# Kernel tuning notes

Hardware: AMD Instinct MI355X
Metric: run time of the kernel (lower is better)

Reference implementation:

```python
import jax, jax.numpy as jnp
import numpy as np

B, S, D, H = 8, 512, 1024, 16
DK = D // H          # 64
N_ASP = 4            # aspect tokens per sample
NEG = -1000000000.0


def setup_inputs() -> dict:
    key = jax.random.key(0)
    ks = jax.random.split(key, 12)
    return {
        "query": jax.random.normal(ks[0], (B, S, D), jnp.float32),
        "key_in": jax.random.normal(ks[1], (B, S, D), jnp.float32),
        "mask": jax.random.randint(ks[2], (B, S, S), 0, 2).astype(jnp.int32),
        "aspect": jax.random.normal(ks[3], (B, 1, D), jnp.float32),
        "aspect_ids": jax.random.randint(ks[4], (B, N_ASP), 0, S),
        # learned params
        "Wq": jax.random.normal(ks[5], (D, D), jnp.float32) / np.sqrt(D).astype(np.float32),
        "bq": jnp.zeros((D,), jnp.float32),
        "Wk": jax.random.normal(ks[6], (D, D), jnp.float32) / np.sqrt(D).astype(np.float32),
        "bk": jnp.zeros((D,), jnp.float32),
        "Wd": jax.random.normal(ks[7], (D, DK), jnp.float32) / np.sqrt(D).astype(np.float32),
        "bd": jnp.zeros((DK,), jnp.float32),
        "weight_m": jax.random.normal(ks[8], (H, DK, DK), jnp.float32) / np.sqrt(DK).astype(np.float32),
        "bias_m": jnp.zeros((1,), jnp.float32),
    }


def reference(query, key_in, mask, aspect, aspect_ids,
              Wq, bq, Wk, bk, Wd, bd, weight_m, bias_m):
    # projections -> [B,H,S,DK]
    q = (query @ Wq + bq).reshape(B, S, H, DK).transpose(0, 2, 1, 3)
    k = (key_in @ Wk + bk).reshape(B, S, H, DK).transpose(0, 2, 1, 3)

    # aspect -> dense -> broadcast to [B,H,S,DK]
    asp = aspect @ Wd + bd                                  # [B,1,DK]
    asp = jnp.broadcast_to(asp[:, None, :, :], (B, H, S, DK))

    # asps = tanh(aspect @ W_m @ K^T + bias_m)  -> [B,H,S,S]
    aw = jnp.einsum('bhsd,hde->bhse', asp, weight_m)
    asps = jnp.tanh(jnp.einsum('bhse,bhte->bhst', aw, k) + bias_m[0])

    # per-(batch,head) average score vector over rows -> [B,H,S]
    avg = asps.sum(axis=-2) / S

    # scatter: for each aspect index, overwrite its row and column with avg
    # (sequential over the small fixed N_ASP, matching torch write order:
    #  row write then column write per index)
    a_sc = asps
    bidx = jnp.arange(B)
    for j in range(N_ASP):
        idx = aspect_ids[:, j]                              # [B]
        a_sc = a_sc.at[bidx, :, idx, :].set(avg)            # rows
        a_sc = a_sc.at[bidx, :, :, idx].set(avg)            # cols

    # standard masked attention probs
    scores = jnp.einsum('bhsd,bhtd->bhst', q, k) / np.float32(np.sqrt(DK))
    scores = jnp.where(mask[:, None, :, :] == 0, NEG, scores)
    attn = jax.nn.softmax(scores, axis=-1)
    return a_sc, attn
```

## Files before the change

### kernel.cpp

```cpp
#include <hip/hip_runtime.h>

typedef __bf16 bf16x8 __attribute__((ext_vector_type(8)));
typedef float  f32x4  __attribute__((ext_vector_type(4)));

__device__ __forceinline__ unsigned short f2bf(float f) {
  union { float f; unsigned u; } x; x.f = f;
  unsigned r = (x.u + 0x7FFFu + ((x.u >> 16) & 1u)) >> 16;
  return (unsigned short)r;
}

__device__ __forceinline__ void gload_lds16(const void* g, void* l) {
  __builtin_amdgcn_global_load_lds((__attribute__((address_space(1))) void*)g,
                                   (__attribute__((address_space(3))) void*)l,
                                   16, 0, 0);
}

__global__ void conv_kernel(const float* __restrict__ a, const float* __restrict__ b,
                            unsigned short* __restrict__ ao, unsigned short* __restrict__ bo,
                            int n4) {
  int i = blockIdx.x * 256 + threadIdx.x;
  if (i < n4) {
    float4 x = ((const float4*)a)[i];
    ushort4 y; y.x = f2bf(x.x); y.y = f2bf(x.y); y.z = f2bf(x.z); y.w = f2bf(x.w);
    ((ushort4*)ao)[i] = y;
  } else {
    int j = i - n4;
    float4 x = ((const float4*)b)[j];
    ushort4 y; y.x = f2bf(x.x); y.y = f2bf(x.y); y.z = f2bf(x.z); y.w = f2bf(x.w);
    ((ushort4*)bo)[j] = y;
  }
}

__global__ void wtrans_kernel(const float* __restrict__ Wq, const float* __restrict__ Wk,
                              unsigned short* __restrict__ Wqt, unsigned short* __restrict__ Wkt) {
  const float* W = blockIdx.z ? Wk : Wq;
  unsigned short* Wt = blockIdx.z ? Wkt : Wqt;
  __shared__ unsigned short tile[32][33];
  int k0 = blockIdx.x * 32, n0 = blockIdx.y * 32;
  int tx = threadIdx.x, ty = threadIdx.y;
  #pragma unroll
  for (int i = 0; i < 4; ++i) {
    int k = ty + i * 8;
    tile[k][tx] = f2bf(W[(size_t)(k0 + k) * 1024 + n0 + tx]);
  }
  __syncthreads();
  #pragma unroll
  for (int i = 0; i < 4; ++i) {
    int n = ty + i * 8;
    Wt[(size_t)(n0 + n) * 1024 + k0 + tx] = tile[tx][n];
  }
}

__global__ __launch_bounds__(256)
void prep_kernel(const float* __restrict__ aspect, const float* __restrict__ Wd,
                 const float* __restrict__ bd, const float* __restrict__ weight_m,
                 const float* __restrict__ Wk, const float* __restrict__ bk,
                 float* __restrict__ u_out, float* __restrict__ c_out) {
  int bh = blockIdx.x, b = bh >> 4, h = bh & 15;
  int tid = threadIdx.x, e = tid & 63, g = tid >> 6;
  __shared__ float part[4][64];
  __shared__ float asp_s[64];
  __shared__ float aw_s[64];
  const float* arow = aspect + (size_t)b * 1024;
  float acc = 0.f;
  for (int d = g * 256; d < g * 256 + 256; ++d)
    acc += arow[d] * Wd[(size_t)d * 64 + e];
  part[g][e] = acc;
  __syncthreads();
  if (tid < 64)
    asp_s[tid] = bd[tid] + part[0][tid] + part[1][tid] + part[2][tid] + part[3][tid];
  __syncthreads();
  if (tid < 64) {
    const float* wm = weight_m + (size_t)h * 4096;
    float aw = 0.f;
    #pragma unroll 8
    for (int d = 0; d < 64; ++d) aw += asp_s[d] * wm[d * 64 + tid];
    aw_s[tid] = aw;
  }
  __syncthreads();
  float awl = aw_s[e];
  if (g == 0) {
    float s = bk[h * 64 + e] * awl;
    #pragma unroll
    for (int off = 32; off >= 1; off >>= 1) s += __shfl_xor(s, off, 64);
    if (e == 0) c_out[bh] = s;
  }
  for (int d0 = g * 2; d0 < 1024; d0 += 8) {
    float s0 = Wk[(size_t)d0 * 1024 + h * 64 + e] * awl;
    float s1 = Wk[(size_t)(d0 + 1) * 1024 + h * 64 + e] * awl;
    #pragma unroll
    for (int off = 32; off >= 1; off >>= 1) {
      s0 += __shfl_xor(s0, off, 64);
      s1 += __shfl_xor(s1, off, 64);
    }
    if (e == 0) {
      u_out[(size_t)bh * 1024 + d0]     = s0;
      u_out[(size_t)bh * 1024 + d0 + 1] = s1;
    }
  }
}

__global__ void bitmask_kernel(const int* __restrict__ mask, unsigned long long* __restrict__ mb) {
  int gw = (blockIdx.x * 256 + threadIdx.x) >> 6;
  int lane = threadIdx.x & 63;
  for (int row = gw; row < 4096; row += 1024) {
    const int* mr = mask + (size_t)row * 512;
    unsigned long long* dst = mb + (size_t)row * 8;
    #pragma unroll
    for (int it = 0; it < 8; ++it) {
      int m = mr[it * 64 + lane];
      unsigned long long bb = __ballot(m != 0);
      if (lane == 0) dst[it] = bb;
    }
  }
}

__global__ __launch_bounds__(256)
void v_kernel(const float* __restrict__ key_in, const float* __restrict__ u,
              const float* __restrict__ c, const float* __restrict__ bias_m,
              float* __restrict__ v) {
  __shared__ float ks_[8][1024];
  int b = blockIdx.y, t0 = blockIdx.x * 8;
  int tid = threadIdx.x, wid = tid >> 6, lane = tid & 63;
  const float4* ksrc = (const float4*)(key_in + ((size_t)b * 512 + t0) * 1024);
  float4* kdst = (float4*)&ks_[0][0];
  for (int i = tid; i < 2048; i += 256) kdst[i] = ksrc[i];
  __syncthreads();
  const float* ub = u + (size_t)b * 16384;
  int r0 = wid * 2;
  float acc0[16] = {}, acc1[16] = {};
  for (int i = 0; i < 16; ++i) {
    int col = lane + 64 * i;
    float kv0 = ks_[r0][col], kv1 = ks_[r0 + 1][col];
    #pragma unroll
    for (int h = 0; h < 16; ++h) {
      float uv = ub[h * 1024 + col];
      acc0[h] += kv0 * uv;
      acc1[h] += kv1 * uv;
    }
  }
  float cb = bias_m[0];
  #pragma unroll
  for (int h = 0; h < 16; ++h) {
    float a0 = acc0[h], a1 = acc1[h];
    #pragma unroll
    for (int off = 32; off >= 1; off >>= 1) {
      a0 += __shfl_xor(a0, off, 64);
      a1 += __shfl_xor(a1, off, 64);
    }
    if (lane == h) {
      int bh = b * 16 + h;
      float cc = c[bh] + cb;
      v[(size_t)bh * 512 + t0 + r0]     = tanhf(a0 + cc);
      v[(size_t)bh * 512 + t0 + r0 + 1] = tanhf(a1 + cc);
    }
  }
}

__global__ void asc_kernel(const float* __restrict__ v, const int* __restrict__ ids,
                           float* __restrict__ out) {
  size_t i4 = (size_t)blockIdx.x * 256 + threadIdx.x;
  int t0 = (int)(i4 & 127) * 4;
  int s  = (int)(i4 >> 7) & 511;
  int bh = (int)(i4 >> 16);
  int b  = bh >> 4;
  int i0 = ids[b * 4], i1 = ids[b * 4 + 1], i2 = ids[b * 4 + 2], i3 = ids[b * 4 + 3];
  #define LASTOF(t) ((i3==(t))?3:(i2==(t))?2:(i1==(t))?1:(i0==(t))?0:-1)
  int ls  = LASTOF(s);
  int lt0 = LASTOF(t0), lt1 = LASTOF(t0+1), lt2 = LASTOF(t0+2), lt3 = LASTOF(t0+3);
  #undef LASTOF
  const float* vrow = v + (size_t)bh * 512;
  float vs = vrow[s];
  float4 vt = *(const float4*)(vrow + t0);
  f32x4 o;
  o[0] = (lt0 >= 0 && lt0 >= ls) ? vs : vt.x;
  o[1] = (lt1 >= 0 && lt1 >= ls) ? vs : vt.y;
  o[2] = (lt2 >= 0 && lt2 >= ls) ? vs : vt.z;
  o[3] = (lt3 >= 0 && lt3 >= ls) ? vs : vt.w;
  __builtin_nontemporal_store(o, ((f32x4*)out) + i4);
}

__global__ __launch_bounds__(256, 2)
void gemm_kernel(const unsigned short* __restrict__ Aq, const unsigned short* __restrict__ Ak,
                 const unsigned short* __restrict__ Bq, const unsigned short* __restrict__ Bk,
                 const float* __restrict__ bq, const float* __restrict__ bk,
                 unsigned short* __restrict__ qb, unsigned short* __restrict__ kb) {
  const unsigned short* A  = blockIdx.z ? Ak : Aq;
  const unsigned short* Bt = blockIdx.z ? Bk : Bq;
  const float* bias = blockIdx.z ? bk : bq;
  unsigned short* out = blockIdx.z ? kb : qb;
  const int m0 = blockIdx.y * 128, n0 = blockIdx.x * 128;
  __shared__ __align__(16) unsigned short As[128 * 32];
  __shared__ __align__(16) unsigned short Bs[128 * 32];
  const int tid = threadIdx.x, wid = tid >> 6, lane = tid & 63;
  const int wr = wid >> 1, wc = wid & 1;
  const int quad = lane >> 4, l15 = lane & 15;
  const int rstage = lane >> 2;
  const int kc = (lane & 3) * 8;
  f32x4 acc[4][4] = {};
  for (int k0 = 0; k0 < 1024; k0 += 32) {
    #pragma unroll
    for (int i = 0; i < 2; ++i) {
      int row = wid * 32 + i * 16 + rstage;
      gload_lds16(A  + (size_t)(m0 + row) * 1024 + k0 + kc, As + (wid * 32 + i * 16) * 32);
      gload_lds16(Bt + (size_t)(n0 + row) * 1024 + k0 + kc, Bs + (wid * 32 + i * 16) * 32);
    }
    __syncthreads();
    bf16x8 af[4], bfr[4];
    #pragma unroll
    for (int mi = 0; mi < 4; ++mi)
      af[mi] = *(const bf16x8*)(As + (wr * 64 + mi * 16 + l15) * 32 + quad * 8);
    #pragma unroll
    for (int ni = 0; ni < 4; ++ni)
      bfr[ni] = *(const bf16x8*)(Bs + (wc * 64 + ni * 16 + l15) * 32 + quad * 8);
    #pragma unroll
    for (int mi = 0; mi < 4; ++mi)
      #pragma unroll
      for (int ni = 0; ni < 4; ++ni)
        acc[mi][ni] = __builtin_amdgcn_mfma_f32_16x16x32_bf16(af[mi], bfr[ni], acc[mi][ni], 0, 0, 0);
    __syncthreads();
  }
  #pragma unroll
  for (int mi = 0; mi < 4; ++mi) {
    #pragma unroll
    for (int ni = 0; ni < 4; ++ni) {
      const int n = n0 + wc * 64 + ni * 16 + l15;
      const int hh = n >> 6, dk = n & 63;
      const float bv = bias[n];
      #pragma unroll
      for (int r = 0; r < 4; ++r) {
        const int m = m0 + wr * 64 + mi * 16 + quad * 4 + r;
        const int bb = m >> 9, ss = m & 511;
        out[(((size_t)bb * 16 + hh) * 512 + ss) * 64 + dk] = f2bf(acc[mi][ni][r] + bv);
      }
    }
  }
}

__global__ __launch_bounds__(256, 2)
void attn_kernel(const unsigned short* __restrict__ qb, const unsigned short* __restrict__ kb,
                 const unsigned* __restrict__ mbits, float* __restrict__ attn) {
  __shared__ __align__(16) unsigned short ks[256 * 64];
  __shared__ __align__(16) unsigned short qs[64 * 64];
  const int s0 = blockIdx.x * 64;
  const int h = blockIdx.y, b = blockIdx.z, bh = b * 16 + h;
  const int tid = threadIdx.x, wid = tid >> 6, lane = tid & 63;
  const int quad = lane >> 4, l15 = lane & 15;
  const unsigned short* kslab = kb + (size_t)bh * 512 * 64;
  const unsigned short* qslab = qb + ((size_t)bh * 512 + s0) * 64;
  #pragma unroll
  for (int i = 0; i < 2; ++i)
    gload_lds16(qslab + (wid * 2 + i) * 512 + lane * 8, qs + (wid * 2 + i) * 512);
  #pragma unroll
  for (int i = 0; i < 8; ++i)
    gload_lds16(kslab + (wid * 8 + i) * 512 + lane * 8, ks + (wid * 8 + i) * 512);
  __syncthreads();
  bf16x8 af0 = *(const bf16x8*)(qs + (wid * 16 + l15) * 64 + quad * 8);
  bf16x8 af1 = *(const bf16x8*)(qs + (wid * 16 + l15) * 64 + 32 + quad * 8);
  f32x4 acc[32];
  #pragma unroll
  for (int tile = 0; tile < 16; ++tile) {
    bf16x8 b0 = *(const bf16x8*)(ks + (tile * 16 + l15) * 64 + quad * 8);
    bf16x8 b1 = *(const bf16x8*)(ks + (tile * 16 + l15) * 64 + 32 + quad * 8);
    f32x4 a = {0.f, 0.f, 0.f, 0.f};
    a = __builtin_amdgcn_mfma_f32_16x16x32_bf16(af0, b0, a, 0, 0, 0);
    a = __builtin_amdgcn_mfma_f32_16x16x32_bf16(af1, b1, a, 0, 0, 0);
    acc[tile] = a;
  }
  __syncthreads();
  #pragma unroll
  for (int i = 0; i < 8; ++i)
    gload_lds16(kslab + 16384 + (wid * 8 + i) * 512 + lane * 8, ks + (wid * 8 + i) * 512);
  __syncthreads();
  #pragma unroll
  for (int tile = 16; tile < 32; ++tile) {
    int tl = tile - 16;
    bf16x8 b0 = *(const bf16x8*)(ks + (tl * 16 + l15) * 64 + quad * 8);
    bf16x8 b1 = *(const bf16x8*)(ks + (tl * 16 + l15) * 64 + 32 + quad * 8);
    f32x4 a = {0.f, 0.f, 0.f, 0.f};
    a = __builtin_amdgcn_mfma_f32_16x16x32_bf16(af0, b0, a, 0, 0, 0);
    a = __builtin_amdgcn_mfma_f32_16x16x32_bf16(af1, b1, a, 0, 0, 0);
    acc[tile] = a;
  }
  const size_t srow = (size_t)s0 + wid * 16 + quad * 4;
  const unsigned* mrow = mbits + ((size_t)b * 512 + srow) * 16;
  float mx[4] = {-3.0e38f, -3.0e38f, -3.0e38f, -3.0e38f};
  #pragma unroll
  for (int tp = 0; tp < 16; ++tp) {
    #pragma unroll
    for (int r = 0; r < 4; ++r) {
      unsigned m = mrow[(size_t)r * 16 + tp];
      float sc0 = acc[2 * tp][r] * 0.125f;
      float sc1 = acc[2 * tp + 1][r] * 0.125f;
      sc0 = ((m >> l15) & 1u) ? sc0 : -1.0e9f;
      sc1 = ((m >> (16 + l15)) & 1u) ? sc1 : -1.0e9f;
      acc[2 * tp][r] = sc0;
      acc[2 * tp + 1][r] = sc1;
      mx[r] = fmaxf(mx[r], fmaxf(sc0, sc1));
    }
  }
  #pragma unroll
  for (int r = 0; r < 4; ++r)
    #pragma unroll
    for (int off = 1; off < 16; off <<= 1)
      mx[r] = fmaxf(mx[r], __shfl_xor(mx[r], off, 64));
  float sm[4] = {0.f, 0.f, 0.f, 0.f};
  #pragma unroll
  for (int tile = 0; tile < 32; ++tile)
    #pragma unroll
    for (int r = 0; r < 4; ++r) {
      float e = __expf(acc[tile][r] - mx[r]);
      acc[tile][r] = e;
      sm[r] += e;
    }
  #pragma unroll
  for (int r = 0; r < 4; ++r) {
    #pragma unroll
    for (int off = 1; off < 16; off <<= 1)
      sm[r] += __shfl_xor(sm[r], off, 64);
    sm[r] = 1.0f / sm[r];
  }
  float* obase = attn + ((size_t)bh * 512 + srow) * 512 + l15;
  #pragma unroll
  for (int r = 0; r < 4; ++r)
    #pragma unroll
    for (int tile = 0; tile < 32; ++tile)
      __builtin_nontemporal_store(acc[tile][r] * sm[r], &obase[(size_t)r * 512 + tile * 16]);
}

extern "C" void kernel_launch(void* const* d_in, const int* in_sizes, int n_in,
                              void* d_out, int out_size, void* d_ws, size_t ws_size,
                              hipStream_t stream) {
  const float* query    = (const float*)d_in[0];
  const float* key_in   = (const float*)d_in[1];
  const int*   mask     = (const int*)d_in[2];
  const float* aspect   = (const float*)d_in[3];
  const int*   a_ids    = (const int*)d_in[4];
  const float* Wq       = (const float*)d_in[5];
  const float* bq       = (const float*)d_in[6];
  const float* Wk       = (const float*)d_in[7];
  const float* bk       = (const float*)d_in[8];
  const float* Wd       = (const float*)d_in[9];
  const float* bd       = (const float*)d_in[10];
  const float* weight_m = (const float*)d_in[11];
  const float* bias_m   = (const float*)d_in[12];

  float* out_asc  = (float*)d_out;
  float* out_attn = out_asc + 33554432ull;

  char* ws = (char*)d_ws;
  unsigned short* Aq   = (unsigned short*)(ws);
  unsigned short* Ak   = (unsigned short*)(ws + 8388608);
  unsigned short* Wqt  = (unsigned short*)(ws + 16777216);
  unsigned short* Wkt  = (unsigned short*)(ws + 18874368);
  unsigned short* qbuf = (unsigned short*)(ws + 20971520);
  unsigned short* kbuf = (unsigned short*)(ws + 29360128);
  float* u   = (float*)(ws + 37748736);
  float* c   = (float*)(ws + 38273024);
  float* v   = (float*)(ws + 38277120);
  unsigned long long* mb = (unsigned long long*)(ws + 38539264);

  conv_kernel<<<dim3(8192), dim3(256), 0, stream>>>(query, key_in, Aq, Ak, 1048576);
  wtrans_kernel<<<dim3(32, 32, 2), dim3(32, 8), 0, stream>>>(Wq, Wk, Wqt, Wkt);
  prep_kernel<<<dim3(128), dim3(256), 0, stream>>>(aspect, Wd, bd, weight_m, Wk, bk, u, c);
  bitmask_kernel<<<dim3(256), dim3(256), 0, stream>>>(mask, mb);
  gemm_kernel<<<dim3(8, 32, 2), dim3(256), 0, stream>>>(Aq, Ak, Wqt, Wkt, bq, bk, qbuf, kbuf);
  v_kernel<<<dim3(64, 8), dim3(256), 0, stream>>>(key_in, u, c, bias_m, v);
  asc_kernel<<<dim3(32768), dim3(256), 0, stream>>>(v, a_ids, out_asc);
  attn_kernel<<<dim3(8, 16, 8), dim3(256), 0, stream>>>(qbuf, kbuf, (const unsigned*)mb, out_attn);
}
```

Baseline: 487.8 us.

## Swizzle LDS layouts, deepen GEMM K-tile, split prep kernel, reorder grids

Splits the serial prep kernel into an aw/c kernel and a separate wide-grid kernel that computes u, so the Wk reduction runs across many blocks instead of 128. The projection GEMM moves to a 64-wide K step with an XOR-swizzled LDS layout to cut bank conflicts and halve the number of barriers. The attention kernel uses the same swizzle for its Q/K tiles. Grid dimensions are reordered in both kernels so blocks that share data run close together. This adds one extra launch and a small workspace buffer, and doubles GEMM LDS use, which may lower occupancy.

```diff
diff --git a/kernel.cpp b/kernel.cpp
--- a/kernel.cpp
+++ b/kernel.cpp
@@ -52,10 +52,10 @@
 }
 
 __global__ __launch_bounds__(256)
-void prep_kernel(const float* __restrict__ aspect, const float* __restrict__ Wd,
-                 const float* __restrict__ bd, const float* __restrict__ weight_m,
-                 const float* __restrict__ Wk, const float* __restrict__ bk,
-                 float* __restrict__ u_out, float* __restrict__ c_out) {
+void prep_aw_kernel(const float* __restrict__ aspect, const float* __restrict__ Wd,
+                    const float* __restrict__ bd, const float* __restrict__ weight_m,
+                    const float* __restrict__ bk,
+                    float* __restrict__ aw_out, float* __restrict__ c_out) {
   int bh = blockIdx.x, b = bh >> 4, h = bh & 15;
   int tid = threadIdx.x, e = tid & 63, g = tid >> 6;
   __shared__ float part[4][64];
@@ -76,16 +76,27 @@
     #pragma unroll 8
     for (int d = 0; d < 64; ++d) aw += asp_s[d] * wm[d * 64 + tid];
     aw_s[tid] = aw;
-  }
-  __syncthreads();
-  float awl = aw_s[e];
+    aw_out[(size_t)bh * 64 + tid] = aw;
+  }
+  __syncthreads();
   if (g == 0) {
-    float s = bk[h * 64 + e] * awl;
+    float s = bk[h * 64 + e] * aw_s[e];
     #pragma unroll
     for (int off = 32; off >= 1; off >>= 1) s += __shfl_xor(s, off, 64);
     if (e == 0) c_out[bh] = s;
   }
-  for (int d0 = g * 2; d0 < 1024; d0 += 8) {
+}
+
+__global__ __launch_bounds__(256)
+void prep_u_kernel(const float* __restrict__ Wk, const float* __restrict__ aw_in,
+                   float* __restrict__ u_out) {
+  int bh = blockIdx.y, h = bh & 15;
+  int dbase = blockIdx.x * 128;
+  int tid = threadIdx.x, e = tid & 63, g = tid >> 6;
+  float awl = aw_in[(size_t)bh * 64 + e];
+  #pragma unroll 4
+  for (int it = 0; it < 16; ++it) {
+    int d0 = dbase + g * 32 + it * 2;
     float s0 = Wk[(size_t)d0 * 1024 + h * 64 + e] * awl;
     float s1 = Wk[(size_t)(d0 + 1) * 1024 + h * 64 + e] * awl;
     #pragma unroll
@@ -189,35 +200,44 @@
   const unsigned short* Bt = blockIdx.z ? Bk : Bq;
   const float* bias = blockIdx.z ? bk : bq;
   unsigned short* out = blockIdx.z ? kb : qb;
-  const int m0 = blockIdx.y * 128, n0 = blockIdx.x * 128;
-  __shared__ __align__(16) unsigned short As[128 * 32];
-  __shared__ __align__(16) unsigned short Bs[128 * 32];
+  const int m0 = blockIdx.x * 128, n0 = blockIdx.y * 128;
+  __shared__ __align__(16) unsigned short As[128 * 64];
+  __shared__ __align__(16) unsigned short Bs[128 * 64];
   const int tid = threadIdx.x, wid = tid >> 6, lane = tid & 63;
   const int wr = wid >> 1, wc = wid & 1;
   const int quad = lane >> 4, l15 = lane & 15;
-  const int rstage = lane >> 2;
-  const int kc = (lane & 3) * 8;
+  const int srw = lane >> 3;
+  const int jcol = ((lane & 7) ^ srw) * 8;
+  const int p0 = (quad ^ (l15 & 7)) * 8;
   f32x4 acc[4][4] = {};
-  for (int k0 = 0; k0 < 1024; k0 += 32) {
-    #pragma unroll
-    for (int i = 0; i < 2; ++i) {
-      int row = wid * 32 + i * 16 + rstage;
-      gload_lds16(A  + (size_t)(m0 + row) * 1024 + k0 + kc, As + (wid * 32 + i * 16) * 32);
-      gload_lds16(Bt + (size_t)(n0 + row) * 1024 + k0 + kc, Bs + (wid * 32 + i * 16) * 32);
+  for (int k0 = 0; k0 < 1024; k0 += 64) {
+    #pragma unroll
+    for (int i = 0; i < 4; ++i) {
+      int r = wid * 32 + i * 8 + srw;
+      gload_lds16(A  + (size_t)(m0 + r) * 1024 + k0 + jcol, As + (wid * 32 + i * 8) * 64);
+      gload_lds16(Bt + (size_t)(n0 + r) * 1024 + k0 + jcol, Bs + (wid * 32 + i * 8) * 64);
     }
     __syncthreads();
-    bf16x8 af[4], bfr[4];
-    #pragma unroll
-    for (int mi = 0; mi < 4; ++mi)
-      af[mi] = *(const bf16x8*)(As + (wr * 64 + mi * 16 + l15) * 32 + quad * 8);
-    #pragma unroll
-    for (int ni = 0; ni < 4; ++ni)
-      bfr[ni] = *(const bf16x8*)(Bs + (wc * 64 + ni * 16 + l15) * 32 + quad * 8);
+    bf16x8 af[4][2], bfr[4][2];
+    #pragma unroll
+    for (int mi = 0; mi < 4; ++mi) {
+      const unsigned short* base = As + (wr * 64 + mi * 16 + l15) * 64;
+      af[mi][0] = *(const bf16x8*)(base + p0);
+      af[mi][1] = *(const bf16x8*)(base + (p0 ^ 32));
+    }
+    #pragma unroll
+    for (int ni = 0; ni < 4; ++ni) {
+      const unsigned short* base = Bs + (wc * 64 + ni * 16 + l15) * 64;
+      bfr[ni][0] = *(const bf16x8*)(base + p0);
+      bfr[ni][1] = *(const bf16x8*)(base + (p0 ^ 32));
+    }
     #pragma unroll
     for (int mi = 0; mi < 4; ++mi)
       #pragma unroll
-      for (int ni = 0; ni < 4; ++ni)
-        acc[mi][ni] = __builtin_amdgcn_mfma_f32_16x16x32_bf16(af[mi], bfr[ni], acc[mi][ni], 0, 0, 0);
+      for (int ni = 0; ni < 4; ++ni) {
+        acc[mi][ni] = __builtin_amdgcn_mfma_f32_16x16x32_bf16(af[mi][0], bfr[ni][0], acc[mi][ni], 0, 0, 0);
+        acc[mi][ni] = __builtin_amdgcn_mfma_f32_16x16x32_bf16(af[mi][1], bfr[ni][1], acc[mi][ni], 0, 0, 0);
+      }
     __syncthreads();
   }
   #pragma unroll
@@ -242,26 +262,31 @@
                  const unsigned* __restrict__ mbits, float* __restrict__ attn) {
   __shared__ __align__(16) unsigned short ks[256 * 64];
   __shared__ __align__(16) unsigned short qs[64 * 64];
-  const int s0 = blockIdx.x * 64;
-  const int h = blockIdx.y, b = blockIdx.z, bh = b * 16 + h;
+  const int bh = blockIdx.x, b = bh >> 4;
+  const int s0 = blockIdx.y * 64;
   const int tid = threadIdx.x, wid = tid >> 6, lane = tid & 63;
   const int quad = lane >> 4, l15 = lane & 15;
+  const int srw = lane >> 3;
+  const int j8 = ((lane & 7) ^ srw) * 8;
+  const int p0 = (quad ^ (l15 & 7)) * 8;
   const unsigned short* kslab = kb + (size_t)bh * 512 * 64;
   const unsigned short* qslab = qb + ((size_t)bh * 512 + s0) * 64;
   #pragma unroll
   for (int i = 0; i < 2; ++i)
-    gload_lds16(qslab + (wid * 2 + i) * 512 + lane * 8, qs + (wid * 2 + i) * 512);
+    gload_lds16(qslab + (wid * 2 + i) * 512 + srw * 64 + j8, qs + (wid * 2 + i) * 512);
   #pragma unroll
   for (int i = 0; i < 8; ++i)
-    gload_lds16(kslab + (wid * 8 + i) * 512 + lane * 8, ks + (wid * 8 + i) * 512);
-  __syncthreads();
-  bf16x8 af0 = *(const bf16x8*)(qs + (wid * 16 + l15) * 64 + quad * 8);
-  bf16x8 af1 = *(const bf16x8*)(qs + (wid * 16 + l15) * 64 + 32 + quad * 8);
+    gload_lds16(kslab + (wid * 8 + i) * 512 + srw * 64 + j8, ks + (wid * 8 + i) * 512);
+  __syncthreads();
+  const unsigned short* qbase = qs + (wid * 16 + l15) * 64;
+  bf16x8 af0 = *(const bf16x8*)(qbase + p0);
+  bf16x8 af1 = *(const bf16x8*)(qbase + (p0 ^ 32));
   f32x4 acc[32];
   #pragma unroll
   for (int tile = 0; tile < 16; ++tile) {
-    bf16x8 b0 = *(const bf16x8*)(ks + (tile * 16 + l15) * 64 + quad * 8);
-    bf16x8 b1 = *(const bf16x8*)(ks + (tile * 16 + l15) * 64 + 32 + quad * 8);
+    const unsigned short* kbase = ks + (tile * 16 + l15) * 64;
+    bf16x8 b0 = *(const bf16x8*)(kbase + p0);
+    bf16x8 b1 = *(const bf16x8*)(kbase + (p0 ^ 32));
     f32x4 a = {0.f, 0.f, 0.f, 0.f};
     a = __builtin_amdgcn_mfma_f32_16x16x32_bf16(af0, b0, a, 0, 0, 0);
     a = __builtin_amdgcn_mfma_f32_16x16x32_bf16(af1, b1, a, 0, 0, 0);
@@ -270,13 +295,13 @@
   __syncthreads();
   #pragma unroll
   for (int i = 0; i < 8; ++i)
-    gload_lds16(kslab + 16384 + (wid * 8 + i) * 512 + lane * 8, ks + (wid * 8 + i) * 512);
+    gload_lds16(kslab + 16384 + (wid * 8 + i) * 512 + srw * 64 + j8, ks + (wid * 8 + i) * 512);
   __syncthreads();
   #pragma unroll
   for (int tile = 16; tile < 32; ++tile) {
-    int tl = tile - 16;
-    bf16x8 b0 = *(const bf16x8*)(ks + (tl * 16 + l15) * 64 + quad * 8);
-    bf16x8 b1 = *(const bf16x8*)(ks + (tl * 16 + l15) * 64 + 32 + quad * 8);
+    const unsigned short* kbase = ks + ((tile - 16) * 16 + l15) * 64;
+    bf16x8 b0 = *(const bf16x8*)(kbase + p0);
+    bf16x8 b1 = *(const bf16x8*)(kbase + (p0 ^ 32));
     f32x4 a = {0.f, 0.f, 0.f, 0.f};
     a = __builtin_amdgcn_mfma_f32_16x16x32_bf16(af0, b0, a, 0, 0, 0);
     a = __builtin_amdgcn_mfma_f32_16x16x32_bf16(af1, b1, a, 0, 0, 0);
@@ -359,13 +384,15 @@
   float* c   = (float*)(ws + 38273024);
   float* v   = (float*)(ws + 38277120);
   unsigned long long* mb = (unsigned long long*)(ws + 38539264);
+  float* aw  = (float*)(ws + 38801408);
 
   conv_kernel<<<dim3(8192), dim3(256), 0, stream>>>(query, key_in, Aq, Ak, 1048576);
   wtrans_kernel<<<dim3(32, 32, 2), dim3(32, 8), 0, stream>>>(Wq, Wk, Wqt, Wkt);
-  prep_kernel<<<dim3(128), dim3(256), 0, stream>>>(aspect, Wd, bd, weight_m, Wk, bk, u, c);
+  prep_aw_kernel<<<dim3(128), dim3(256), 0, stream>>>(aspect, Wd, bd, weight_m, bk, aw, c);
   bitmask_kernel<<<dim3(256), dim3(256), 0, stream>>>(mask, mb);
-  gemm_kernel<<<dim3(8, 32, 2), dim3(256), 0, stream>>>(Aq, Ak, Wqt, Wkt, bq, bk, qbuf, kbuf);
+  prep_u_kernel<<<dim3(8, 128), dim3(256), 0, stream>>>(Wk, aw, u);
+  gemm_kernel<<<dim3(32, 8, 2), dim3(256), 0, stream>>>(Aq, Ak, Wqt, Wkt, bq, bk, qbuf, kbuf);
   v_kernel<<<dim3(64, 8), dim3(256), 0, stream>>>(key_in, u, c, bias_m, v);
   asc_kernel<<<dim3(32768), dim3(256), 0, stream>>>(v, a_ids, out_asc);
-  attn_kernel<<<dim3(8, 16, 8), dim3(256), 0, stream>>>(qbuf, kbuf, (const unsigned*)mb, out_attn);
-}
+  attn_kernel<<<dim3(128, 8), dim3(256), 0, stream>>>(qbuf, kbuf, (const unsigned*)mb, out_attn);
+}
```

Measured after the change: 425.2 us. 12.8% less time.
